# Kernel optimization log

Measured on AMD Instinct MI355X. Metric: run time of the kernel, lower is better.

## Reference

```python
import jax, jax.numpy as jnp
import numpy as np

EMB_SCALE = 0.001  # embedding_scale when normalize=False


def setup_inputs() -> dict:
    key = jax.random.key(0)
    k1, k2 = jax.random.split(key)
    N, S, C, V, K = 8, 4096, 2, 128, 512
    x0 = jax.random.normal(k1, (N, S, C, V), dtype=jnp.float32)
    embedding = jax.random.normal(k2, (C, K, V), dtype=jnp.float32) * EMB_SCALE
    return {"x0": x0, "embedding": embedding}


def reference(x0, embedding):
    # normalize=False path: x = x0, embedding used as-is
    N, S, C, V = x0.shape
    K = embedding.shape[1]
    x = x0
    xf = x.reshape(N * S, C, V)  # (B, C, V), B = N*S tokens

    # (the ||x||^2 term is constant over k). Avoids materializing (B, C, K, V).
    dots = jnp.einsum('bcv,ckv->bck', xf, embedding)          # (B, C, K)
    e_sq = jnp.sum(embedding * embedding, axis=2)             # (C, K)
    dist2 = e_sq[None, :, :] - 2.0 * dots                     # (B, C, K)
    index = jnp.argmin(dist2, axis=2)                         # (B, C) int

    # Entropy of codebook usage (original divides by len(index) == B rows)
    B = N * S
    hist = jnp.bincount(index.reshape(-1), length=K).astype(jnp.float32)
    prob = hist / jnp.float32(B)
    entropy = -jnp.sum(jnp.where(hist > 0, prob * jnp.log(jnp.maximum(prob, 1e-30)), 0.0))

    # Gather: output[b, c] = embedding[c, index[b, c]]
    output = embedding[jnp.arange(C), index]                  # (B, C, V)
    output = output.reshape(N, S, C, V)

    out0 = jax.lax.stop_gradient(output - x) + x              # straight-through
    out1 = jnp.sum((jax.lax.stop_gradient(x) - output) ** 2, axis=3)  # (N,S,C)
    out2 = (jnp.sum((x - jax.lax.stop_gradient(output)) ** 2, axis=3)
            + jnp.sum((x - x0) ** 2, axis=3))                 # (N,S,C); (x-x0)==0 here
    return (out0, out1, out2, entropy)
```

## Files before the change

kernel.cpp:

```cpp
#include <hip/hip_runtime.h>
#include <math.h>

#define N_TOK   32768
#define C_CH    2
#define V_DIM   128
#define K_CODES 512
#define TPB     128
#define BAND    4.0e-3f

typedef short     bf16v8 __attribute__((ext_vector_type(8)));
typedef float     f32x4  __attribute__((ext_vector_type(4)));
typedef unsigned  u32x4  __attribute__((ext_vector_type(4)));
typedef __attribute__((address_space(1))) const unsigned char* gas_t;
typedef __attribute__((address_space(3))) unsigned char* las_t;

__device__ inline unsigned f2bf(float f) {
    unsigned u = __float_as_uint(f);
    return (u + 0x7FFFu + ((u >> 16) & 1u)) >> 16;
}

__global__ __launch_bounds__(64) void vq_prep(const float* __restrict__ emb,
                                              float* __restrict__ e_sq,
                                              unsigned int* __restrict__ hist,
                                              unsigned char* __restrict__ img) {
    const int row  = blockIdx.x;
    const int k    = row & (K_CODES - 1);
    const int lane = threadIdx.x;
    const float a = emb[(size_t)row * V_DIM + lane];
    const float b = emb[(size_t)row * V_DIM + 64 + lane];
    float s = a * a + b * b;
#pragma unroll
    for (int off = 32; off; off >>= 1) s += __shfl_down(s, off);
    if (lane == 0) {
        e_sq[row] = s;
        if (row < K_CODES) hist[row] = 0u;
    }
    if (lane < 16) {
        const int sp = lane;
        const int sl = sp ^ (k & 7);
        const float* src = emb + (size_t)row * V_DIM + sl * 8;
        u32x4 val;
#pragma unroll
        for (int q = 0; q < 4; ++q)
            val[q] = f2bf(src[2 * q]) | (f2bf(src[2 * q + 1]) << 16);
        *reinterpret_cast<u32x4*>(img + ((size_t)row * 16 + sp) * 16) = val;
    }
}

__global__ __launch_bounds__(256, 2) void vq_main(const float* __restrict__ x0,
                                                  const float* __restrict__ emb,
                                                  const float* __restrict__ e_sq,
                                                  const unsigned char* __restrict__ img,
                                                  unsigned int* __restrict__ hist,
                                                  float* __restrict__ out0,
                                                  float* __restrict__ out1,
                                                  float* __restrict__ out2) {
    __shared__ __align__(16) unsigned char xs[TPB * 256];
    __shared__ __align__(16) unsigned char es[128 * 256];
    __shared__ float esq_s[K_CODES];
    __shared__ float xx_s[TPB];
    __shared__ unsigned long long best_s[TPB];
    __shared__ unsigned int cand[1024];
    __shared__ int cand_n;

    const int c    = blockIdx.y;
    const int gt0  = blockIdx.x * TPB;
    const int t    = threadIdx.x;
    const int lane = t & 63;
    const int w    = t >> 6;
    const int l15  = lane & 15;
    const int l4   = lane >> 4;

    if (t < TPB) best_s[t] = ~0ull;
    if (t == 0) cand_n = 0;
    esq_s[t]       = e_sq[c * K_CODES + t];
    esq_s[t + 256] = e_sq[c * K_CODES + t + 256];

    {
        const int row  = t >> 1;
        const int half = t & 1;
        const float* xp = x0 + ((size_t)(gt0 + row) * C_CH + c) * V_DIM + half * 64;
        float xxp = 0.f;
#pragma unroll
        for (int q = 0; q < 8; ++q) {
            f32x4 p0 = *reinterpret_cast<const f32x4*>(xp + q * 8);
            f32x4 p1 = *reinterpret_cast<const f32x4*>(xp + q * 8 + 4);
            xxp = fmaf(p0[0], p0[0], xxp); xxp = fmaf(p0[1], p0[1], xxp);
            xxp = fmaf(p0[2], p0[2], xxp); xxp = fmaf(p0[3], p0[3], xxp);
            xxp = fmaf(p1[0], p1[0], xxp); xxp = fmaf(p1[1], p1[1], xxp);
            xxp = fmaf(p1[2], p1[2], xxp); xxp = fmaf(p1[3], p1[3], xxp);
            u32x4 val;
            val[0] = f2bf(p0[0]) | (f2bf(p0[1]) << 16);
            val[1] = f2bf(p0[2]) | (f2bf(p0[3]) << 16);
            val[2] = f2bf(p1[0]) | (f2bf(p1[1]) << 16);
            val[3] = f2bf(p1[2]) | (f2bf(p1[3]) << 16);
            const int sp = (half * 8 + q) ^ (row & 7);
            *reinterpret_cast<u32x4*>(xs + (size_t)row * 256 + sp * 16) = val;
        }
        xxp += __shfl_xor(xxp, 1);
        if (half == 0) xx_s[row] = xxp;
    }
    __syncthreads();

    u32x4 Af[2][4];
#pragma unroll
    for (int m = 0; m < 2; ++m)
#pragma unroll
        for (int kk = 0; kk < 4; ++kk) {
            const int row = w * 32 + m * 16 + l15;
            const int sp  = (kk * 4 + l4) ^ (row & 7);
            Af[m][kk] = *reinterpret_cast<const u32x4*>(xs + (size_t)row * 256 + sp * 16);
        }

    float rmin[2][4];
#pragma unroll
    for (int m = 0; m < 2; ++m)
#pragma unroll
        for (int r = 0; r < 4; ++r) rmin[m][r] = INFINITY;

    for (int sweep = 0; sweep < 2; ++sweep) {
        for (int Q = 0; Q < 4; ++Q) {
            __syncthreads();
            const unsigned char* src = img + (size_t)(c * K_CODES + Q * 128) * 256;
#pragma unroll
            for (int i = 0; i < 8; ++i) {
                const int chunk = i * 256 + w * 64;
                __builtin_amdgcn_global_load_lds(
                    (gas_t)(src + (size_t)(chunk + lane) * 16),
                    (las_t)(es + (size_t)chunk * 16), 16, 0, 0);
            }
            __syncthreads();

            for (int j = 0; j < 8; ++j) {
                f32x4 acc0 = {0.f, 0.f, 0.f, 0.f};
                f32x4 acc1 = {0.f, 0.f, 0.f, 0.f};
                const int code = j * 16 + l15;
#pragma unroll
                for (int kk = 0; kk < 4; ++kk) {
                    const int sp = (kk * 4 + l4) ^ (code & 7);
                    bf16v8 B = __builtin_bit_cast(bf16v8,
                        *reinterpret_cast<const u32x4*>(es + (size_t)code * 256 + sp * 16));
                    acc0 = __builtin_amdgcn_mfma_f32_16x16x32_bf16(
                        __builtin_bit_cast(bf16v8, Af[0][kk]), B, acc0, 0, 0, 0);
                    acc1 = __builtin_amdgcn_mfma_f32_16x16x32_bf16(
                        __builtin_bit_cast(bf16v8, Af[1][kk]), B, acc1, 0, 0, 0);
                }
                const int   kglob = Q * 128 + code;
                const float esv   = esq_s[kglob];
                if (sweep == 0) {
#pragma unroll
                    for (int r = 0; r < 4; ++r) {
                        rmin[0][r] = fminf(rmin[0][r], fmaf(-2.f, acc0[r], esv));
                        rmin[1][r] = fminf(rmin[1][r], fmaf(-2.f, acc1[r], esv));
                    }
                } else {
#pragma unroll
                    for (int m = 0; m < 2; ++m)
#pragma unroll
                        for (int r = 0; r < 4; ++r) {
                            const float d = fmaf(-2.f, (m ? acc1[r] : acc0[r]), esv);
                            if (d <= rmin[m][r] + BAND) {
                                const int tok = w * 32 + m * 16 + l4 * 4 + r;
                                const int pos = atomicAdd(&cand_n, 1);
                                if (pos < 1024)
                                    cand[pos] = ((unsigned)tok << 9) | (unsigned)kglob;
                            }
                        }
                }
            }
        }
        if (sweep == 0) {
#pragma unroll
            for (int m = 0; m < 2; ++m)
#pragma unroll
                for (int r = 0; r < 4; ++r) {
                    float v = rmin[m][r];
#pragma unroll
                    for (int s = 1; s < 16; s <<= 1) v = fminf(v, __shfl_xor(v, s));
                    rmin[m][r] = v;
                }
        }
    }

    __syncthreads();
    const int n = cand_n < 1024 ? cand_n : 1024;
    for (int i = t; i < n; i += 256) {
        const unsigned key = cand[i];
        const int tok = key >> 9;
        const int k   = key & (K_CODES - 1);
        const float* xg = x0 + ((size_t)(gt0 + tok) * C_CH + c) * V_DIM;
        const float* eg = emb + ((size_t)c * K_CODES + k) * V_DIM;
        float a0 = 0.f, a1 = 0.f, a2 = 0.f, a3 = 0.f;
#pragma unroll
        for (int q = 0; q < 32; ++q) {
            f32x4 xv = *reinterpret_cast<const f32x4*>(xg + q * 4);
            f32x4 ev = *reinterpret_cast<const f32x4*>(eg + q * 4);
            a0 = fmaf(xv[0], ev[0], a0);
            a1 = fmaf(xv[1], ev[1], a1);
            a2 = fmaf(xv[2], ev[2], a2);
            a3 = fmaf(xv[3], ev[3], a3);
        }
        const float dot = (a0 + a1) + (a2 + a3);
        const float d   = fmaf(-2.f, dot, esq_s[k]);
        unsigned u = __float_as_uint(d);
        u = ((int)u < 0) ? ~u : (u | 0x80000000u);
        atomicMin(&best_s[tok], ((unsigned long long)u << 32) | (unsigned)k);
    }
    __syncthreads();

    if (t < TPB) {
        const unsigned long long b = best_s[t];
        const int k = (int)(b & (unsigned)(K_CODES - 1));
        const unsigned u = (unsigned)(b >> 32);
        const float d = __uint_as_float((u & 0x80000000u) ? (u & 0x7FFFFFFFu) : ~u);
        const float o12 = xx_s[t] + d;
        const size_t oi = (size_t)(gt0 + t) * C_CH + c;
        out1[oi] = o12;
        out2[oi] = o12;
        atomicAdd(&hist[k], 1u);
    }

#pragma unroll
    for (int i = 0; i < 16; ++i) {
        const int tok = i * 8 + (t >> 5);
        const int v4  = t & 31;
        const int k   = (int)(best_s[tok] & (unsigned long long)(K_CODES - 1));
        const float* eg = emb + ((size_t)c * K_CODES + k) * V_DIM + v4 * 4;
        const float* xg = x0 + ((size_t)(gt0 + tok) * C_CH + c) * V_DIM + v4 * 4;
        f32x4 ev = *reinterpret_cast<const f32x4*>(eg);
        f32x4 xv = *reinterpret_cast<const f32x4*>(xg);
        f32x4 ov;
#pragma unroll
        for (int z = 0; z < 4; ++z) ov[z] = (ev[z] - xv[z]) + xv[z];
        *reinterpret_cast<f32x4*>(out0 + ((size_t)(gt0 + tok) * C_CH + c) * V_DIM + v4 * 4) = ov;
    }
}

__global__ __launch_bounds__(512) void vq_entropy(const unsigned int* __restrict__ hist,
                                                  float* __restrict__ ent) {
    const int t = threadIdx.x;
    float v = 0.f;
    const unsigned int h = hist[t];
    if (h > 0u) {
        const float p = (float)h * (1.0f / 32768.0f);
        v = p * logf(p);
    }
#pragma unroll
    for (int off = 32; off; off >>= 1) v += __shfl_down(v, off);
    __shared__ float s[8];
    if ((t & 63) == 0) s[t >> 6] = v;
    __syncthreads();
    if (t == 0) {
        float tot = 0.f;
#pragma unroll
        for (int i = 0; i < 8; ++i) tot += s[i];
        ent[0] = -tot;
    }
}

extern "C" void kernel_launch(void* const* d_in, const int* in_sizes, int n_in,
                              void* d_out, int out_size, void* d_ws, size_t ws_size,
                              hipStream_t stream) {
    const float* x0  = (const float*)d_in[0];
    const float* emb = (const float*)d_in[1];

    float*         e_sq = (float*)d_ws;
    unsigned int*  hist = (unsigned int*)((char*)d_ws + 4096);
    unsigned char* img  = (unsigned char*)d_ws + 8192;

    float* out0 = (float*)d_out;
    float* out1 = out0 + (size_t)N_TOK * C_CH * V_DIM;
    float* out2 = out1 + (size_t)N_TOK * C_CH;
    float* ent  = out2 + (size_t)N_TOK * C_CH;

    vq_prep<<<C_CH * K_CODES, 64, 0, stream>>>(emb, e_sq, hist, img);
    vq_main<<<dim3(N_TOK / TPB, C_CH), 256, 0, stream>>>(x0, emb, e_sq, img, hist,
                                                         out0, out1, out2);
    vq_entropy<<<1, K_CODES, 0, stream>>>(hist, ent);
}
```

Baseline: 76.37 us.

## Split codebook across waves with per-wave double-buffered staging and fp32 x tile

Each block now handles 64 tokens instead of 128. Each of its four waves covers all 64 tokens against its own quarter of the codebook, so the B-operand tiles are staged per wave. Staging uses double-buffered global_load_lds with explicit vmcnt waits instead of block-wide barriers. The x tile is kept in LDS as fp32 so the refinement and output phases read x from LDS rather than global memory, and the per-token minimum is combined across waves through a shared atomicMin. The change doubles the grid and adds cross-wave reduction, and it relies on hand-placed waitcnt and sched_barrier for correctness.

```diff
diff --git a/kernel.cpp b/kernel.cpp
--- a/kernel.cpp
+++ b/kernel.cpp
@@ -5,7 +5,7 @@
 #define C_CH    2
 #define V_DIM   128
 #define K_CODES 512
-#define TPB     128
+#define TPB     64
 #define BAND    4.0e-3f
 
 typedef short     bf16v8 __attribute__((ext_vector_type(8)));
@@ -14,9 +14,21 @@
 typedef __attribute__((address_space(1))) const unsigned char* gas_t;
 typedef __attribute__((address_space(3))) unsigned char* las_t;
 
+#define WAITV(n) do { asm volatile("s_waitcnt vmcnt(" #n ")" ::: "memory"); \
+                      __builtin_amdgcn_sched_barrier(0); } while (0)
+#define WAITL()  do { asm volatile("s_waitcnt lgkmcnt(0)" ::: "memory");    \
+                      __builtin_amdgcn_sched_barrier(0); } while (0)
+
 __device__ inline unsigned f2bf(float f) {
     unsigned u = __float_as_uint(f);
     return (u + 0x7FFFu + ((u >> 16) & 1u)) >> 16;
+}
+__device__ inline unsigned mapf(float d) {
+    unsigned u = __float_as_uint(d);
+    return ((int)u < 0) ? ~u : (u | 0x80000000u);
+}
+__device__ inline float unmapf(unsigned u) {
+    return __uint_as_float((u & 0x80000000u) ? (u & 0x7FFFFFFFu) : ~u);
 }
 
 __global__ __launch_bounds__(64) void vq_prep(const float* __restrict__ emb,
@@ -55,10 +67,12 @@
                                                   float* __restrict__ out0,
                                                   float* __restrict__ out1,
                                                   float* __restrict__ out2) {
-    __shared__ __align__(16) unsigned char xs[TPB * 256];
-    __shared__ __align__(16) unsigned char es[128 * 256];
+    __shared__ __align__(16) float xs[TPB * 132];
+    __shared__ __align__(16) unsigned char esA[4][4096];
+    __shared__ __align__(16) unsigned char esB[4][4096];
     __shared__ float esq_s[K_CODES];
     __shared__ float xx_s[TPB];
+    __shared__ unsigned int dmin_s[TPB];
     __shared__ unsigned long long best_s[TPB];
     __shared__ unsigned int cand[1024];
     __shared__ int cand_n;
@@ -71,148 +85,165 @@
     const int l15  = lane & 15;
     const int l4   = lane >> 4;
 
-    if (t < TPB) best_s[t] = ~0ull;
+#pragma unroll
+    for (int it = 0; it < 8; ++it) {
+        const int row = it * 8 + w * 2 + (lane >> 5);
+        const int col = (lane & 31) * 4;
+        const f32x4 xv = *reinterpret_cast<const f32x4*>(
+            x0 + ((size_t)(gt0 + row) * C_CH + c) * V_DIM + col);
+        *reinterpret_cast<f32x4*>(&xs[row * 132 + col]) = xv;
+        float part = xv[0] * xv[0] + xv[1] * xv[1] + xv[2] * xv[2] + xv[3] * xv[3];
+#pragma unroll
+        for (int m2 = 1; m2 <= 16; m2 <<= 1) part += __shfl_xor(part, m2);
+        if ((lane & 31) == 0) xx_s[row] = part;
+    }
+    esq_s[t]       = e_sq[c * K_CODES + t];
+    esq_s[t + 256] = e_sq[c * K_CODES + 256 + t];
+    if (t < TPB) { best_s[t] = ~0ull; dmin_s[t] = 0xFFFFFFFFu; }
     if (t == 0) cand_n = 0;
-    esq_s[t]       = e_sq[c * K_CODES + t];
-    esq_s[t + 256] = e_sq[c * K_CODES + t + 256];
-
-    {
-        const int row  = t >> 1;
-        const int half = t & 1;
-        const float* xp = x0 + ((size_t)(gt0 + row) * C_CH + c) * V_DIM + half * 64;
-        float xxp = 0.f;
-#pragma unroll
-        for (int q = 0; q < 8; ++q) {
-            f32x4 p0 = *reinterpret_cast<const f32x4*>(xp + q * 8);
-            f32x4 p1 = *reinterpret_cast<const f32x4*>(xp + q * 8 + 4);
-            xxp = fmaf(p0[0], p0[0], xxp); xxp = fmaf(p0[1], p0[1], xxp);
-            xxp = fmaf(p0[2], p0[2], xxp); xxp = fmaf(p0[3], p0[3], xxp);
-            xxp = fmaf(p1[0], p1[0], xxp); xxp = fmaf(p1[1], p1[1], xxp);
-            xxp = fmaf(p1[2], p1[2], xxp); xxp = fmaf(p1[3], p1[3], xxp);
-            u32x4 val;
-            val[0] = f2bf(p0[0]) | (f2bf(p0[1]) << 16);
-            val[1] = f2bf(p0[2]) | (f2bf(p0[3]) << 16);
-            val[2] = f2bf(p1[0]) | (f2bf(p1[1]) << 16);
-            val[3] = f2bf(p1[2]) | (f2bf(p1[3]) << 16);
-            const int sp = (half * 8 + q) ^ (row & 7);
-            *reinterpret_cast<u32x4*>(xs + (size_t)row * 256 + sp * 16) = val;
-        }
-        xxp += __shfl_xor(xxp, 1);
-        if (half == 0) xx_s[row] = xxp;
-    }
-    __syncthreads();
-
-    u32x4 Af[2][4];
-#pragma unroll
-    for (int m = 0; m < 2; ++m)
+    __syncthreads();
+
+    u32x4 Af[4][4];
+#pragma unroll
+    for (int m = 0; m < 4; ++m)
 #pragma unroll
         for (int kk = 0; kk < 4; ++kk) {
-            const int row = w * 32 + m * 16 + l15;
-            const int sp  = (kk * 4 + l4) ^ (row & 7);
-            Af[m][kk] = *reinterpret_cast<const u32x4*>(xs + (size_t)row * 256 + sp * 16);
-        }
-
-    float rmin[2][4];
-#pragma unroll
-    for (int m = 0; m < 2; ++m)
+            const float* xr = &xs[(m * 16 + l15) * 132 + kk * 32 + l4 * 8];
+            const f32x4 lo = *reinterpret_cast<const f32x4*>(xr);
+            const f32x4 hi = *reinterpret_cast<const f32x4*>(xr + 4);
+            u32x4 v;
+            v[0] = f2bf(lo[0]) | (f2bf(lo[1]) << 16);
+            v[1] = f2bf(lo[2]) | (f2bf(lo[3]) << 16);
+            v[2] = f2bf(hi[0]) | (f2bf(hi[1]) << 16);
+            v[3] = f2bf(hi[2]) | (f2bf(hi[3]) << 16);
+            Af[m][kk] = v;
+        }
+
+    unsigned char* bA = esA[w];
+    unsigned char* bB = esB[w];
+    const unsigned char* imgc = img + ((size_t)c * K_CODES) * 256;
+
+    auto STAGE = [&](unsigned char* buf, int chunk) {
+        const unsigned char* src = imgc + (size_t)(w * 128 + chunk * 16) * 256;
+#pragma unroll
+        for (int p = 0; p < 4; ++p)
+            __builtin_amdgcn_global_load_lds(
+                (gas_t)(src + (size_t)(p * 64 + lane) * 16),
+                (las_t)(buf + p * 1024), 16, 0, 0);
+    };
+
+    float rmin[4][4];
+#pragma unroll
+    for (int m = 0; m < 4; ++m)
 #pragma unroll
         for (int r = 0; r < 4; ++r) rmin[m][r] = INFINITY;
-
-    for (int sweep = 0; sweep < 2; ++sweep) {
-        for (int Q = 0; Q < 4; ++Q) {
-            __syncthreads();
-            const unsigned char* src = img + (size_t)(c * K_CODES + Q * 128) * 256;
-#pragma unroll
-            for (int i = 0; i < 8; ++i) {
-                const int chunk = i * 256 + w * 64;
-                __builtin_amdgcn_global_load_lds(
-                    (gas_t)(src + (size_t)(chunk + lane) * 16),
-                    (las_t)(es + (size_t)chunk * 16), 16, 0, 0);
-            }
-            __syncthreads();
-
-            for (int j = 0; j < 8; ++j) {
-                f32x4 acc0 = {0.f, 0.f, 0.f, 0.f};
-                f32x4 acc1 = {0.f, 0.f, 0.f, 0.f};
-                const int code = j * 16 + l15;
-#pragma unroll
-                for (int kk = 0; kk < 4; ++kk) {
-                    const int sp = (kk * 4 + l4) ^ (code & 7);
-                    bf16v8 B = __builtin_bit_cast(bf16v8,
-                        *reinterpret_cast<const u32x4*>(es + (size_t)code * 256 + sp * 16));
-                    acc0 = __builtin_amdgcn_mfma_f32_16x16x32_bf16(
-                        __builtin_bit_cast(bf16v8, Af[0][kk]), B, acc0, 0, 0, 0);
-                    acc1 = __builtin_amdgcn_mfma_f32_16x16x32_bf16(
-                        __builtin_bit_cast(bf16v8, Af[1][kk]), B, acc1, 0, 0, 0);
+    float dminv[4][4];
+
+    auto COMPUTE = [&](const unsigned char* buf, int chunk, bool collect) {
+        const int kglob = w * 128 + chunk * 16 + l15;
+        f32x4 acc[4] = {{0.f,0.f,0.f,0.f},{0.f,0.f,0.f,0.f},
+                        {0.f,0.f,0.f,0.f},{0.f,0.f,0.f,0.f}};
+#pragma unroll
+        for (int kk = 0; kk < 4; ++kk) {
+            const int sp = (kk * 4 + l4) ^ (kglob & 7);
+            const bf16v8 B = __builtin_bit_cast(bf16v8,
+                *reinterpret_cast<const u32x4*>(buf + l15 * 256 + sp * 16));
+#pragma unroll
+            for (int m = 0; m < 4; ++m)
+                acc[m] = __builtin_amdgcn_mfma_f32_16x16x32_bf16(
+                    __builtin_bit_cast(bf16v8, Af[m][kk]), B, acc[m], 0, 0, 0);
+        }
+        const float esv = esq_s[kglob];
+        if (!collect) {
+#pragma unroll
+            for (int m = 0; m < 4; ++m)
+#pragma unroll
+                for (int r = 0; r < 4; ++r)
+                    rmin[m][r] = fminf(rmin[m][r], fmaf(-2.f, acc[m][r], esv));
+        } else {
+#pragma unroll
+            for (int m = 0; m < 4; ++m)
+#pragma unroll
+                for (int r = 0; r < 4; ++r) {
+                    const float d = fmaf(-2.f, acc[m][r], esv);
+                    if (d <= dminv[m][r]) {
+                        const int tok = m * 16 + l4 * 4 + r;
+                        const int pos = atomicAdd(&cand_n, 1);
+                        if (pos < 1024)
+                            cand[pos] = ((unsigned)tok << 9) | (unsigned)kglob;
+                    }
                 }
-                const int   kglob = Q * 128 + code;
-                const float esv   = esq_s[kglob];
-                if (sweep == 0) {
-#pragma unroll
-                    for (int r = 0; r < 4; ++r) {
-                        rmin[0][r] = fminf(rmin[0][r], fmaf(-2.f, acc0[r], esv));
-                        rmin[1][r] = fminf(rmin[1][r], fmaf(-2.f, acc1[r], esv));
-                    }
-                } else {
-#pragma unroll
-                    for (int m = 0; m < 2; ++m)
-#pragma unroll
-                        for (int r = 0; r < 4; ++r) {
-                            const float d = fmaf(-2.f, (m ? acc1[r] : acc0[r]), esv);
-                            if (d <= rmin[m][r] + BAND) {
-                                const int tok = w * 32 + m * 16 + l4 * 4 + r;
-                                const int pos = atomicAdd(&cand_n, 1);
-                                if (pos < 1024)
-                                    cand[pos] = ((unsigned)tok << 9) | (unsigned)kglob;
-                            }
-                        }
-                }
-            }
-        }
-        if (sweep == 0) {
-#pragma unroll
-            for (int m = 0; m < 2; ++m)
-#pragma unroll
-                for (int r = 0; r < 4; ++r) {
-                    float v = rmin[m][r];
-#pragma unroll
-                    for (int s = 1; s < 16; s <<= 1) v = fminf(v, __shfl_xor(v, s));
-                    rmin[m][r] = v;
-                }
-        }
-    }
-
-    __syncthreads();
+        }
+    };
+
+#define SWEEP(collect)                                                    \
+    do {                                                                  \
+        STAGE(bA, 0);                                                     \
+        STAGE(bB, 1);                                                     \
+        WAITV(4); COMPUTE(bA, 0, collect);                                \
+        WAITL();  STAGE(bA, 2);                                           \
+        WAITV(4); COMPUTE(bB, 1, collect);                                \
+        WAITL();  STAGE(bB, 3);                                           \
+        WAITV(4); COMPUTE(bA, 2, collect);                                \
+        WAITL();  STAGE(bA, 4);                                           \
+        WAITV(4); COMPUTE(bB, 3, collect);                                \
+        WAITL();  STAGE(bB, 5);                                           \
+        WAITV(4); COMPUTE(bA, 4, collect);                                \
+        WAITL();  STAGE(bA, 6);                                           \
+        WAITV(4); COMPUTE(bB, 5, collect);                                \
+        WAITL();  STAGE(bB, 7);                                           \
+        WAITV(4); COMPUTE(bA, 6, collect);                                \
+        WAITV(0); COMPUTE(bB, 7, collect);                                \
+    } while (0)
+
+    SWEEP(false);
+
+#pragma unroll
+    for (int m = 0; m < 4; ++m)
+#pragma unroll
+        for (int r = 0; r < 4; ++r) {
+            float v = rmin[m][r];
+#pragma unroll
+            for (int s = 1; s < 16; s <<= 1) v = fminf(v, __shfl_xor(v, s));
+            if (l15 == 0) atomicMin(&dmin_s[m * 16 + l4 * 4 + r], mapf(v));
+        }
+    __syncthreads();
+#pragma unroll
+    for (int m = 0; m < 4; ++m)
+#pragma unroll
+        for (int r = 0; r < 4; ++r)
+            dminv[m][r] = unmapf(dmin_s[m * 16 + l4 * 4 + r]) + BAND;
+
+    SWEEP(true);
+    __syncthreads();
+
     const int n = cand_n < 1024 ? cand_n : 1024;
     for (int i = t; i < n; i += 256) {
         const unsigned key = cand[i];
         const int tok = key >> 9;
-        const int k   = key & (K_CODES - 1);
-        const float* xg = x0 + ((size_t)(gt0 + tok) * C_CH + c) * V_DIM;
-        const float* eg = emb + ((size_t)c * K_CODES + k) * V_DIM;
+        const int kc  = key & (K_CODES - 1);
+        const float* xg = &xs[tok * 132];
+        const float* eg = emb + ((size_t)c * K_CODES + kc) * V_DIM;
         float a0 = 0.f, a1 = 0.f, a2 = 0.f, a3 = 0.f;
 #pragma unroll
         for (int q = 0; q < 32; ++q) {
-            f32x4 xv = *reinterpret_cast<const f32x4*>(xg + q * 4);
-            f32x4 ev = *reinterpret_cast<const f32x4*>(eg + q * 4);
+            const f32x4 xv = *reinterpret_cast<const f32x4*>(xg + q * 4);
+            const f32x4 ev = *reinterpret_cast<const f32x4*>(eg + q * 4);
             a0 = fmaf(xv[0], ev[0], a0);
             a1 = fmaf(xv[1], ev[1], a1);
             a2 = fmaf(xv[2], ev[2], a2);
             a3 = fmaf(xv[3], ev[3], a3);
         }
         const float dot = (a0 + a1) + (a2 + a3);
-        const float d   = fmaf(-2.f, dot, esq_s[k]);
-        unsigned u = __float_as_uint(d);
-        u = ((int)u < 0) ? ~u : (u | 0x80000000u);
-        atomicMin(&best_s[tok], ((unsigned long long)u << 32) | (unsigned)k);
+        const float d   = fmaf(-2.f, dot, esq_s[kc]);
+        atomicMin(&best_s[tok], ((unsigned long long)mapf(d) << 32) | (unsigned)kc);
     }
     __syncthreads();
 
     if (t < TPB) {
         const unsigned long long b = best_s[t];
         const int k = (int)(b & (unsigned)(K_CODES - 1));
-        const unsigned u = (unsigned)(b >> 32);
-        const float d = __uint_as_float((u & 0x80000000u) ? (u & 0x7FFFFFFFu) : ~u);
+        const float d = unmapf((unsigned)(b >> 32));
         const float o12 = xx_s[t] + d;
         const size_t oi = (size_t)(gt0 + t) * C_CH + c;
         out1[oi] = o12;
@@ -221,18 +252,18 @@
     }
 
 #pragma unroll
-    for (int i = 0; i < 16; ++i) {
+    for (int i = 0; i < 8; ++i) {
         const int tok = i * 8 + (t >> 5);
         const int v4  = t & 31;
         const int k   = (int)(best_s[tok] & (unsigned long long)(K_CODES - 1));
-        const float* eg = emb + ((size_t)c * K_CODES + k) * V_DIM + v4 * 4;
-        const float* xg = x0 + ((size_t)(gt0 + tok) * C_CH + c) * V_DIM + v4 * 4;
-        f32x4 ev = *reinterpret_cast<const f32x4*>(eg);
-        f32x4 xv = *reinterpret_cast<const f32x4*>(xg);
+        const f32x4 ev = *reinterpret_cast<const f32x4*>(
+            emb + ((size_t)c * K_CODES + k) * V_DIM + v4 * 4);
+        const f32x4 xv = *reinterpret_cast<const f32x4*>(&xs[tok * 132 + v4 * 4]);
         f32x4 ov;
 #pragma unroll
         for (int z = 0; z < 4; ++z) ov[z] = (ev[z] - xv[z]) + xv[z];
-        *reinterpret_cast<f32x4*>(out0 + ((size_t)(gt0 + tok) * C_CH + c) * V_DIM + v4 * 4) = ov;
+        *reinterpret_cast<f32x4*>(
+            out0 + ((size_t)(gt0 + tok) * C_CH + c) * V_DIM + v4 * 4) = ov;
     }
 }
 
```

Result: slower. 88.75 us (+16.2%).

## Shrink token tile to 32, split codes across waves, single-pass distance search

Applied to the files above, without the earlier changes.

Each block now handles 32 tokens instead of 128. The four waves split the 512 codes among themselves rather than splitting tokens, and all distances are kept in registers so the codebook is streamed once instead of twice. The per-token minimum is combined across waves with LDS atomics before candidates are collected, and occupancy is raised to 3 blocks per CU. The risks are heavier register pressure from the 64-float distance array, four times as many blocks each reloading the full 512-code bf16 image, and candidates being silently dropped by the smaller 512-entry buffer.

```diff
diff --git a/kernel.cpp b/kernel.cpp
--- a/kernel.cpp
+++ b/kernel.cpp
@@ -1,12 +1,13 @@
 #include <hip/hip_runtime.h>
 #include <math.h>
 
-#define N_TOK   32768
-#define C_CH    2
-#define V_DIM   128
-#define K_CODES 512
-#define TPB     128
-#define BAND    4.0e-3f
+#define N_TOK    32768
+#define C_CH     2
+#define V_DIM    128
+#define K_CODES  512
+#define TPB      32
+#define CAND_CAP 512
+#define BAND     4.0e-3f
 
 typedef short     bf16v8 __attribute__((ext_vector_type(8)));
 typedef float     f32x4  __attribute__((ext_vector_type(4)));
@@ -17,6 +18,13 @@
 __device__ inline unsigned f2bf(float f) {
     unsigned u = __float_as_uint(f);
     return (u + 0x7FFFu + ((u >> 16) & 1u)) >> 16;
+}
+__device__ inline unsigned mapf(float d) {
+    unsigned u = __float_as_uint(d);
+    return ((int)u < 0) ? ~u : (u | 0x80000000u);
+}
+__device__ inline float unmapf(unsigned u) {
+    return __uint_as_float((u & 0x80000000u) ? (u & 0x7FFFFFFFu) : ~u);
 }
 
 __global__ __launch_bounds__(64) void vq_prep(const float* __restrict__ emb,
@@ -47,7 +55,7 @@
     }
 }
 
-__global__ __launch_bounds__(256, 2) void vq_main(const float* __restrict__ x0,
+__global__ __launch_bounds__(256, 3) void vq_main(const float* __restrict__ x0,
                                                   const float* __restrict__ emb,
                                                   const float* __restrict__ e_sq,
                                                   const unsigned char* __restrict__ img,
@@ -55,12 +63,12 @@
                                                   float* __restrict__ out0,
                                                   float* __restrict__ out1,
                                                   float* __restrict__ out2) {
+    __shared__ __align__(16) unsigned char es[128 * 256];
     __shared__ __align__(16) unsigned char xs[TPB * 256];
-    __shared__ __align__(16) unsigned char es[128 * 256];
-    __shared__ float esq_s[K_CODES];
     __shared__ float xx_s[TPB];
+    __shared__ unsigned int dmin_s[TPB];
     __shared__ unsigned long long best_s[TPB];
-    __shared__ unsigned int cand[1024];
+    __shared__ unsigned int cand[CAND_CAP];
     __shared__ int cand_n;
 
     const int c    = blockIdx.y;
@@ -71,35 +79,50 @@
     const int l15  = lane & 15;
     const int l4   = lane >> 4;
 
-    if (t < TPB) best_s[t] = ~0ull;
+    if (t < TPB) { dmin_s[t] = 0xFFFFFFFFu; best_s[t] = ~0ull; }
     if (t == 0) cand_n = 0;
-    esq_s[t]       = e_sq[c * K_CODES + t];
-    esq_s[t + 256] = e_sq[c * K_CODES + t + 256];
 
     {
-        const int row  = t >> 1;
-        const int half = t & 1;
-        const float* xp = x0 + ((size_t)(gt0 + row) * C_CH + c) * V_DIM + half * 64;
-        float xxp = 0.f;
-#pragma unroll
-        for (int q = 0; q < 8; ++q) {
-            f32x4 p0 = *reinterpret_cast<const f32x4*>(xp + q * 8);
-            f32x4 p1 = *reinterpret_cast<const f32x4*>(xp + q * 8 + 4);
-            xxp = fmaf(p0[0], p0[0], xxp); xxp = fmaf(p0[1], p0[1], xxp);
-            xxp = fmaf(p0[2], p0[2], xxp); xxp = fmaf(p0[3], p0[3], xxp);
-            xxp = fmaf(p1[0], p1[0], xxp); xxp = fmaf(p1[1], p1[1], xxp);
-            xxp = fmaf(p1[2], p1[2], xxp); xxp = fmaf(p1[3], p1[3], xxp);
-            u32x4 val;
-            val[0] = f2bf(p0[0]) | (f2bf(p0[1]) << 16);
-            val[1] = f2bf(p0[2]) | (f2bf(p0[3]) << 16);
-            val[2] = f2bf(p1[0]) | (f2bf(p1[1]) << 16);
-            val[3] = f2bf(p1[2]) | (f2bf(p1[3]) << 16);
-            const int sp = (half * 8 + q) ^ (row & 7);
-            *reinterpret_cast<u32x4*>(xs + (size_t)row * 256 + sp * 16) = val;
-        }
-        xxp += __shfl_xor(xxp, 1);
-        if (half == 0) xx_s[row] = xxp;
-    }
+        const int row = t >> 3;
+        const int q   = t & 7;
+        const float* xp = x0 + ((size_t)(gt0 + row) * C_CH + c) * V_DIM + q * 16;
+        f32x4 p0 = *reinterpret_cast<const f32x4*>(xp);
+        f32x4 p1 = *reinterpret_cast<const f32x4*>(xp + 4);
+        f32x4 p2 = *reinterpret_cast<const f32x4*>(xp + 8);
+        f32x4 p3 = *reinterpret_cast<const f32x4*>(xp + 12);
+        float part = 0.f;
+#pragma unroll
+        for (int z = 0; z < 4; ++z) {
+            part = fmaf(p0[z], p0[z], part);
+            part = fmaf(p1[z], p1[z], part);
+            part = fmaf(p2[z], p2[z], part);
+            part = fmaf(p3[z], p3[z], part);
+        }
+#pragma unroll
+        for (int m2 = 1; m2 <= 4; m2 <<= 1) part += __shfl_xor(part, m2);
+        if (q == 0) xx_s[row] = part;
+        u32x4 v0, v1;
+        v0[0] = f2bf(p0[0]) | (f2bf(p0[1]) << 16);
+        v0[1] = f2bf(p0[2]) | (f2bf(p0[3]) << 16);
+        v0[2] = f2bf(p1[0]) | (f2bf(p1[1]) << 16);
+        v0[3] = f2bf(p1[2]) | (f2bf(p1[3]) << 16);
+        v1[0] = f2bf(p2[0]) | (f2bf(p2[1]) << 16);
+        v1[1] = f2bf(p2[2]) | (f2bf(p2[3]) << 16);
+        v1[2] = f2bf(p3[0]) | (f2bf(p3[1]) << 16);
+        v1[3] = f2bf(p3[2]) | (f2bf(p3[3]) << 16);
+        const int s0 = (q * 2)     ^ (row & 7);
+        const int s1 = (q * 2 + 1) ^ (row & 7);
+        *reinterpret_cast<u32x4*>(xs + row * 256 + s0 * 16) = v0;
+        *reinterpret_cast<u32x4*>(xs + row * 256 + s1 * 16) = v1;
+    }
+
+    float esq_r[8];
+#pragma unroll
+    for (int Q = 0; Q < 4; ++Q)
+#pragma unroll
+        for (int n = 0; n < 2; ++n)
+            esq_r[Q * 2 + n] = e_sq[c * K_CODES + Q * 128 + w * 32 + n * 16 + l15];
+
     __syncthreads();
 
     u32x4 Af[2][4];
@@ -107,112 +130,115 @@
     for (int m = 0; m < 2; ++m)
 #pragma unroll
         for (int kk = 0; kk < 4; ++kk) {
-            const int row = w * 32 + m * 16 + l15;
-            const int sp  = (kk * 4 + l4) ^ (row & 7);
-            Af[m][kk] = *reinterpret_cast<const u32x4*>(xs + (size_t)row * 256 + sp * 16);
-        }
-
-    float rmin[2][4];
+            const int row = m * 16 + l15;
+            Af[m][kk] = *reinterpret_cast<const u32x4*>(
+                xs + row * 256 + (((kk * 4 + l4) ^ (row & 7)) * 16));
+        }
+
+    float dt[2][8][4];
+    const unsigned char* imgc = img + ((size_t)c * K_CODES) * 256;
+
+#pragma unroll
+    for (int Q = 0; Q < 4; ++Q) {
+        __syncthreads();
+        {
+            const unsigned char* src = imgc + (size_t)Q * 128 * 256;
+#pragma unroll
+            for (int i = 0; i < 8; ++i) {
+                const int off = (i * 4 + w) * 1024;
+                __builtin_amdgcn_global_load_lds(
+                    (gas_t)(src + off + lane * 16),
+                    (las_t)(es + off), 16, 0, 0);
+            }
+        }
+        __syncthreads();
+
+#pragma unroll
+        for (int n = 0; n < 2; ++n) {
+            const int row = w * 32 + n * 16 + l15;
+            u32x4 B[4];
+#pragma unroll
+            for (int kk = 0; kk < 4; ++kk)
+                B[kk] = *reinterpret_cast<const u32x4*>(
+                    es + row * 256 + (((kk * 4 + l4) ^ (row & 7)) * 16));
+            f32x4 a0 = {0.f, 0.f, 0.f, 0.f};
+            f32x4 a1 = {0.f, 0.f, 0.f, 0.f};
+#pragma unroll
+            for (int kk = 0; kk < 4; ++kk) {
+                a0 = __builtin_amdgcn_mfma_f32_16x16x32_bf16(
+                    __builtin_bit_cast(bf16v8, Af[0][kk]),
+                    __builtin_bit_cast(bf16v8, B[kk]), a0, 0, 0, 0);
+                a1 = __builtin_amdgcn_mfma_f32_16x16x32_bf16(
+                    __builtin_bit_cast(bf16v8, Af[1][kk]),
+                    __builtin_bit_cast(bf16v8, B[kk]), a1, 0, 0, 0);
+            }
+            const float esv = esq_r[Q * 2 + n];
+#pragma unroll
+            for (int r = 0; r < 4; ++r) {
+                dt[0][Q * 2 + n][r] = fmaf(-2.f, a0[r], esv);
+                dt[1][Q * 2 + n][r] = fmaf(-2.f, a1[r], esv);
+            }
+        }
+    }
+
 #pragma unroll
     for (int m = 0; m < 2; ++m)
 #pragma unroll
-        for (int r = 0; r < 4; ++r) rmin[m][r] = INFINITY;
-
-    for (int sweep = 0; sweep < 2; ++sweep) {
-        for (int Q = 0; Q < 4; ++Q) {
-            __syncthreads();
-            const unsigned char* src = img + (size_t)(c * K_CODES + Q * 128) * 256;
-#pragma unroll
-            for (int i = 0; i < 8; ++i) {
-                const int chunk = i * 256 + w * 64;
-                __builtin_amdgcn_global_load_lds(
-                    (gas_t)(src + (size_t)(chunk + lane) * 16),
-                    (las_t)(es + (size_t)chunk * 16), 16, 0, 0);
-            }
-            __syncthreads();
-
-            for (int j = 0; j < 8; ++j) {
-                f32x4 acc0 = {0.f, 0.f, 0.f, 0.f};
-                f32x4 acc1 = {0.f, 0.f, 0.f, 0.f};
-                const int code = j * 16 + l15;
-#pragma unroll
-                for (int kk = 0; kk < 4; ++kk) {
-                    const int sp = (kk * 4 + l4) ^ (code & 7);
-                    bf16v8 B = __builtin_bit_cast(bf16v8,
-                        *reinterpret_cast<const u32x4*>(es + (size_t)code * 256 + sp * 16));
-                    acc0 = __builtin_amdgcn_mfma_f32_16x16x32_bf16(
-                        __builtin_bit_cast(bf16v8, Af[0][kk]), B, acc0, 0, 0, 0);
-                    acc1 = __builtin_amdgcn_mfma_f32_16x16x32_bf16(
-                        __builtin_bit_cast(bf16v8, Af[1][kk]), B, acc1, 0, 0, 0);
-                }
-                const int   kglob = Q * 128 + code;
-                const float esv   = esq_s[kglob];
-                if (sweep == 0) {
-#pragma unroll
-                    for (int r = 0; r < 4; ++r) {
-                        rmin[0][r] = fminf(rmin[0][r], fmaf(-2.f, acc0[r], esv));
-                        rmin[1][r] = fminf(rmin[1][r], fmaf(-2.f, acc1[r], esv));
-                    }
-                } else {
-#pragma unroll
-                    for (int m = 0; m < 2; ++m)
-#pragma unroll
-                        for (int r = 0; r < 4; ++r) {
-                            const float d = fmaf(-2.f, (m ? acc1[r] : acc0[r]), esv);
-                            if (d <= rmin[m][r] + BAND) {
-                                const int tok = w * 32 + m * 16 + l4 * 4 + r;
-                                const int pos = atomicAdd(&cand_n, 1);
-                                if (pos < 1024)
-                                    cand[pos] = ((unsigned)tok << 9) | (unsigned)kglob;
-                            }
-                        }
+        for (int r = 0; r < 4; ++r) {
+            float v = dt[m][0][r];
+#pragma unroll
+            for (int qn = 1; qn < 8; ++qn) v = fminf(v, dt[m][qn][r]);
+#pragma unroll
+            for (int s = 1; s < 16; s <<= 1) v = fminf(v, __shfl_xor(v, s));
+            if (l15 == 0) atomicMin(&dmin_s[m * 16 + l4 * 4 + r], mapf(v));
+        }
+    __syncthreads();
+
+#pragma unroll
+    for (int m = 0; m < 2; ++m)
+#pragma unroll
+        for (int r = 0; r < 4; ++r) {
+            const int tok = m * 16 + l4 * 4 + r;
+            const float thr = unmapf(dmin_s[tok]) + BAND;
+#pragma unroll
+            for (int qn = 0; qn < 8; ++qn) {
+                if (dt[m][qn][r] <= thr) {
+                    const int k = (qn >> 1) * 128 + w * 32 + (qn & 1) * 16 + l15;
+                    const int pos = atomicAdd(&cand_n, 1);
+                    if (pos < CAND_CAP)
+                        cand[pos] = ((unsigned)tok << 9) | (unsigned)k;
                 }
             }
         }
-        if (sweep == 0) {
-#pragma unroll
-            for (int m = 0; m < 2; ++m)
-#pragma unroll
-                for (int r = 0; r < 4; ++r) {
-                    float v = rmin[m][r];
-#pragma unroll
-                    for (int s = 1; s < 16; s <<= 1) v = fminf(v, __shfl_xor(v, s));
-                    rmin[m][r] = v;
-                }
-        }
-    }
-
-    __syncthreads();
-    const int n = cand_n < 1024 ? cand_n : 1024;
-    for (int i = t; i < n; i += 256) {
+    __syncthreads();
+
+    const int nc = cand_n < CAND_CAP ? cand_n : CAND_CAP;
+    for (int i = t; i < nc; i += 256) {
         const unsigned key = cand[i];
         const int tok = key >> 9;
-        const int k   = key & (K_CODES - 1);
+        const int kc  = key & (K_CODES - 1);
         const float* xg = x0 + ((size_t)(gt0 + tok) * C_CH + c) * V_DIM;
-        const float* eg = emb + ((size_t)c * K_CODES + k) * V_DIM;
+        const float* eg = emb + ((size_t)c * K_CODES + kc) * V_DIM;
         float a0 = 0.f, a1 = 0.f, a2 = 0.f, a3 = 0.f;
-#pragma unroll
+#pragma unroll 4
         for (int q = 0; q < 32; ++q) {
-            f32x4 xv = *reinterpret_cast<const f32x4*>(xg + q * 4);
-            f32x4 ev = *reinterpret_cast<const f32x4*>(eg + q * 4);
+            const f32x4 xv = *reinterpret_cast<const f32x4*>(xg + q * 4);
+            const f32x4 ev = *reinterpret_cast<const f32x4*>(eg + q * 4);
             a0 = fmaf(xv[0], ev[0], a0);
             a1 = fmaf(xv[1], ev[1], a1);
             a2 = fmaf(xv[2], ev[2], a2);
             a3 = fmaf(xv[3], ev[3], a3);
         }
         const float dot = (a0 + a1) + (a2 + a3);
-        const float d   = fmaf(-2.f, dot, esq_s[k]);
-        unsigned u = __float_as_uint(d);
-        u = ((int)u < 0) ? ~u : (u | 0x80000000u);
-        atomicMin(&best_s[tok], ((unsigned long long)u << 32) | (unsigned)k);
+        const float d   = fmaf(-2.f, dot, e_sq[c * K_CODES + kc]);
+        atomicMin(&best_s[tok], ((unsigned long long)mapf(d) << 32) | (unsigned)kc);
     }
     __syncthreads();
 
     if (t < TPB) {
         const unsigned long long b = best_s[t];
         const int k = (int)(b & (unsigned)(K_CODES - 1));
-        const unsigned u = (unsigned)(b >> 32);
-        const float d = __uint_as_float((u & 0x80000000u) ? (u & 0x7FFFFFFFu) : ~u);
+        const float d = unmapf((unsigned)(b >> 32));
         const float o12 = xx_s[t] + d;
         const size_t oi = (size_t)(gt0 + t) * C_CH + c;
         out1[oi] = o12;
@@ -221,18 +247,19 @@
     }
 
 #pragma unroll
-    for (int i = 0; i < 16; ++i) {
+    for (int i = 0; i < 4; ++i) {
         const int tok = i * 8 + (t >> 5);
         const int v4  = t & 31;
         const int k   = (int)(best_s[tok] & (unsigned long long)(K_CODES - 1));
-        const float* eg = emb + ((size_t)c * K_CODES + k) * V_DIM + v4 * 4;
-        const float* xg = x0 + ((size_t)(gt0 + tok) * C_CH + c) * V_DIM + v4 * 4;
-        f32x4 ev = *reinterpret_cast<const f32x4*>(eg);
-        f32x4 xv = *reinterpret_cast<const f32x4*>(xg);
+        const f32x4 ev = *reinterpret_cast<const f32x4*>(
+            emb + ((size_t)c * K_CODES + k) * V_DIM + v4 * 4);
+        const f32x4 xv = *reinterpret_cast<const f32x4*>(
+            x0 + ((size_t)(gt0 + tok) * C_CH + c) * V_DIM + v4 * 4);
         f32x4 ov;
 #pragma unroll
         for (int z = 0; z < 4; ++z) ov[z] = (ev[z] - xv[z]) + xv[z];
-        *reinterpret_cast<f32x4*>(out0 + ((size_t)(gt0 + tok) * C_CH + c) * V_DIM + v4 * 4) = ov;
+        *reinterpret_cast<f32x4*>(
+            out0 + ((size_t)(gt0 + tok) * C_CH + c) * V_DIM + v4 * 4) = ov;
     }
 }
 
```

After: 74.45 us. -2.5%, faster.
